# Kernel optimization log

Measured on AMD Instinct MI355X. Metric: run time of the kernel, lower is better.

The kernel has to match this reference:

```python
import jax, jax.numpy as jnp
import numpy as np

PS = 7        # pooled_size == conved_size
IMG = 300     # img_size
FMAP = 19     # feature map spatial size
SMAX = IMG // 16  # clamp max (18), matches torch long clamp(0, 300/16)
EPS = 1e-5


def _bn(x, g, b, m, v):
    scale = (g * jax.lax.rsqrt(v + EPS))[None, :, None, None]
    return x * scale + (b - m * g * jax.lax.rsqrt(v + EPS))[None, :, None, None]


def _conv(x, W, b=None, pad=1):
    y = jax.lax.conv_general_dilated(x, W, (1, 1), [(pad, pad), (pad, pad)],
                                     dimension_numbers=('NCHW', 'OIHW', 'NCHW'))
    if b is not None:
        y = y + b[None, :, None, None]
    return y


def _adaptive_w(lo, hi):
    # Per-ROI adaptive-avg-pool weights over the full 19-wide axis.
    # lo, hi: [B,R] inclusive crop bounds. Returns [B,R,PS,FMAP].
    H = hi - lo + 1                                  # crop length per ROI
    i = jnp.arange(PS)
    s = (i[None, None, :] * H[..., None]) // PS      # bin start (floor)
    e = -((-(i[None, None, :] + 1) * H[..., None]) // PS)  # bin end (ceil)
    rows = jnp.arange(FMAP)
    start = lo[..., None, None] + s[..., None]
    stop = lo[..., None, None] + e[..., None]
    mask = (rows >= start) & (rows < stop)
    denom = jnp.maximum(e - s, 1).astype(jnp.float32)[..., None]
    return mask.astype(jnp.float32) / denom


def setup_inputs() -> dict:
    key = jax.random.key(0)
    ks = jax.random.split(key, 6)
    B, R = 8, 128
    return {
        'roi_proposal': jax.random.uniform(ks[0], (B, 1, R, 5), dtype=jnp.float32),
        'features': jax.random.normal(ks[1], (B, 1024, FMAP, FMAP), dtype=jnp.float32),
        'W1': jax.random.normal(ks[2], (256, 1024, 3, 3), dtype=jnp.float32) * 0.02,
        'b1': jnp.zeros((256,), jnp.float32),
        'g1': jnp.ones((256,), jnp.float32),
        'be1': jnp.zeros((256,), jnp.float32),
        'm1': jnp.zeros((256,), jnp.float32),
        'v1': jnp.ones((256,), jnp.float32),
        'W2': jax.random.normal(ks[3], (256, 256, 3, 3), jnp.float32) * 0.05,
        'b2': jnp.zeros((256,), jnp.float32),
        'g2': jnp.ones((256,), jnp.float32),
        'be2': jnp.zeros((256,), jnp.float32),
        'm2': jnp.zeros((256,), jnp.float32),
        'v2': jnp.ones((256,), jnp.float32),
        'W3': jax.random.normal(ks[4], (32, 256, 1, 1), jnp.float32) * 0.1,
        'g3': jnp.ones((32,), jnp.float32),
        'be3': jnp.zeros((32,), jnp.float32),
        'm3': jnp.zeros((32,), jnp.float32),
        'v3': jnp.ones((32,), jnp.float32),
    }


def reference(roi_proposal, features, W1, b1, g1, be1, m1, v1,
              W2, b2, g2, be2, m2, v2, W3, g3, be3, m3, v3):
    # rois[..., 1:] * img_size / 16, then trunc to long (coords are >= 0)
    rl = (roi_proposal[:, 0, :, 1:] * (IMG / 16.0)).astype(jnp.int32)  # [B,R,4]
    c = jnp.clip(rl, 0, SMAX)
    xmin, ymin, xmax, ymax = c[..., 0], c[..., 1], c[..., 2], c[..., 3]
    valid = (xmax > xmin) & (ymax > ymin)                              # [B,R]
    B, R = valid.shape

    # fused crop + adaptive avg pool as two small pooling matmuls per ROI
    Wy = _adaptive_w(ymin, ymax)   # [B,R,7,19]
    Wx = _adaptive_w(xmin, xmax)   # [B,R,7,19]
    pooled = jnp.einsum('brph,bchw,brqw->brcpq', Wy, features, Wx)     # [B,R,1024,7,7]

    x = pooled.reshape(B * R, 1024, PS, PS)
    x = jax.nn.relu(_bn(_conv(x, W1, b1), g1, be1, m1, v1))
    x = jax.nn.relu(_bn(_conv(x, W2, b2), g2, be2, m2, v2))
    x = jax.nn.relu(_bn(_conv(x, W3, None, pad=0), g3, be3, m3, v3))
    out = x.reshape(B, R, 32, PS, PS) * valid[:, :, None, None, None]

    # compact valid ROIs to the front per batch (stable), invalid slots zeroed
    perm = jnp.argsort((~valid).astype(jnp.int32), axis=1, stable=True)
    out_c = jax.vmap(lambda o, p: o[p])(out, perm)                     # [B,R,32,7,7]
    er = rl.astype(jnp.float32) * (16.0 / IMG) * valid[..., None]
    er_c = jax.vmap(lambda o, p: o[p])(er, perm)[:, None]              # [B,1,R,4]
    keep_count = valid.sum(axis=1).astype(jnp.int32)                   # [B]
    return er_c, out_c, keep_count
```

## Files before the change

### kernel.cpp

```cpp
#include <hip/hip_runtime.h>
#include <cstddef>
#include <cstdint>

typedef unsigned short u16;
typedef unsigned int u32;
typedef __attribute__((ext_vector_type(8))) short short8;
typedef __attribute__((ext_vector_type(4))) float f32x4;

#define NB 8
#define NR 128
#define NPOS 49
#define EPSV 1e-5f
#define NSLOT 512

#define OUT_OC   4096
#define OUT_KEEP 1609728

static constexpr size_t OFF_META = 256;
static constexpr size_t OFF_KEEP = 33024;
static constexpr size_t OFF_W1Q  = 40960;
static constexpr size_t OFF_W2Q  = OFF_W1Q + 4718592;
static constexpr size_t OFF_W3   = OFF_W2Q + 1179648;
static constexpr size_t OFF_X1S  = OFF_W3  + 32768;
static constexpr size_t OFF_AP   = OFF_X1S + 13107200;
static constexpr size_t WS_NEED  = OFF_AP  + 51380224;

static __device__ __forceinline__ u16 f2bf(float f) {
  union { float f; u32 u; } x; x.f = f;
  u32 r = 0x7fffu + ((x.u >> 16) & 1u);
  return (u16)((x.u + r) >> 16);
}

__global__ void k_setup(const float* __restrict__ roi, int* __restrict__ cnt,
                        int* __restrict__ meta, int* __restrict__ keepd,
                        float* __restrict__ out)
{
  int b = blockIdx.x, t = threadIdx.x;
  __shared__ int sval[128], spre[129];
  const float* rp = roi + (size_t)(b * NR + t) * 5;
  int rl[4], cl[4];
#pragma unroll
  for (int j = 0; j < 4; ++j) {
    rl[j] = (int)(rp[1 + j] * 18.75f);
    cl[j] = min(max(rl[j], 0), 18);
  }
  int valid = (cl[2] > cl[0]) && (cl[3] > cl[1]) ? 1 : 0;
  sval[t] = valid;
  __syncthreads();
  if (t == 0) {
    int s = 0;
    for (int i = 0; i < 128; ++i) { spre[i] = s; s += sval[i]; }
    spre[128] = s;
    keepd[b] = s;
    out[OUT_KEEP + b] = (float)s;
  }
  __syncthreads();
  int keep = spre[128];
  if (valid) {
    int dst = spre[t];
    int slot = atomicAdd(cnt, 1);
    int* mt = meta + slot * 8;
    mt[0] = b; mt[1] = dst;
    mt[2] = cl[1]; mt[3] = cl[3];
    mt[4] = cl[0]; mt[5] = cl[2];
#pragma unroll
    for (int j = 0; j < 4; ++j)
      out[(size_t)(b * NR + dst) * 4 + j] = (float)rl[j] * (16.0f / 300.0f);
  }
  if (t >= keep) {
#pragma unroll
    for (int j = 0; j < 4; ++j) out[(size_t)(b * NR + t) * 4 + j] = 0.f;
  }
}

__global__ __launch_bounds__(256) void k_int(const float* __restrict__ feat, float* __restrict__ S)
{
  int b = blockIdx.x, cg = blockIdx.y;
  __shared__ float F[64 * 361];
  int tid = threadIdx.x;
  const float* fb = feat + ((size_t)b * 1024 + cg * 64) * 361;
#pragma unroll 1
  for (int i = tid; i < 64 * 361; i += 256) F[i] = fb[i];
  __syncthreads();
  if (tid < 64) {
    int ch = tid;
    const float* fp = F + ch * 361;
    float* Sp = S + (size_t)b * 400 * 1024 + cg * 64 + ch;
    float prev[20];
#pragma unroll
    for (int w = 0; w < 20; ++w) { prev[w] = 0.f; Sp[(size_t)w * 1024] = 0.f; }
    for (int h = 0; h < 19; ++h) {
      float run = 0.f;
      float* Sr = Sp + (size_t)(h + 1) * 20 * 1024;
      Sr[0] = 0.f;
#pragma unroll
      for (int w = 0; w < 19; ++w) {
        run += fp[h * 19 + w];
        float v = run + prev[w + 1];
        Sr[(size_t)(w + 1) * 1024] = v;
        prev[w + 1] = v;
      }
    }
  }
}

__device__ __forceinline__ void packw_body(const float* __restrict__ W, u16* __restrict__ wq,
                                           int IC, int c, int og)
{
  __shared__ float F[32 * 576];
  int tid = threadIdx.x, oc0 = og * 32;
#pragma unroll 1
  for (int i = tid; i < 18432; i += 256) {
    int ocr = i / 576, r = i - ocr * 576;
    F[i] = W[(size_t)(oc0 + ocr) * IC * 9 + c * 576 + r];
  }
  __syncthreads();
#pragma unroll 1
  for (int w = tid; w < 18432; w += 256) {
    int j = w & 7, lane = (w >> 3) & 63, rest = w >> 9;
    int ntr = rest & 1, kk = rest >> 1;
    int k9i = kk >> 1, ks = kk & 1;
    int ocr = ntr * 16 + (lane & 15);
    int icr = ks * 32 + ((lane >> 4) & 3) * 8 + j;
    int bid_ = (c * 9 + k9i) * 2 + ks;
    wq[((size_t)bid_ * 1024 + (oc0 / 16 + ntr) * 64 + lane) * 8 + j] = f2bf(F[ocr * 576 + icr * 9 + k9i]);
  }
}
__global__ __launch_bounds__(256) void k_prep(
    const float* __restrict__ W1, const float* __restrict__ W2, const float* __restrict__ W3,
    u16* __restrict__ w1q, u16* __restrict__ w2q, u16* __restrict__ w3q)
{
  if (blockIdx.z == 0) { packw_body(W1, w1q, 1024, blockIdx.x, blockIdx.y); return; }
  if (blockIdx.x < 4)  { packw_body(W2, w2q, 256, blockIdx.x, blockIdx.y); return; }
  if (blockIdx.x == 4 && blockIdx.y == 0) {
    for (int i = threadIdx.x; i < 8192; i += 256) {
      int oc = i >> 8, ic = i & 255;
      int kk = ic >> 5;
      int lane = ((ic >> 3) & 3) * 16 + (oc & 15);
      int nt16 = oc >> 4;
      int j = ic & 7;
      w3q[((size_t)((kk * 2 + nt16) * 64) + lane) * 8 + j] = f2bf(W3[i]);
    }
  }
}

__global__ __launch_bounds__(256) void k_pool(
    const int* __restrict__ cnt, const int* __restrict__ meta,
    const float* __restrict__ S, u16* __restrict__ Apool)
{
  int cv = *cnt; if (cv > NSLOT) cv = NSLOT;
  int slot = blockIdx.x;
  if (slot >= cv) return;
  const int* mt_ = meta + slot * 8;
  int b = mt_[0], ylo = mt_[2], yhi = mt_[3], xlo = mt_[4], xhi = mt_[5];
  int Hy = yhi - ylo + 1, Hx = xhi - xlo + 1;
  const float* Sb = S + (size_t)b * 400 * 1024;
  u16* Ap = Apool + (size_t)slot * 50176;
  int base = blockIdx.y * 25088, end = base + 25088;
  int tid = threadIdx.x;
#pragma unroll 1
  for (int t0 = base + tid; t0 < end; t0 += 1024) {
#pragma unroll
    for (int u = 0; u < 4; ++u) {
      int t = t0 + u * 256;
      if (t < end) {
        int ch = t & 63, r = t >> 6;
        int bin = r % 49, c = r / 49;
        int p = bin / 7, q = bin - 7 * p;
        int sy = (p * Hy) / 7, ey = ((p + 1) * Hy + 6) / 7;
        int sx = (q * Hx) / 7, ex = ((q + 1) * Hx + 6) / 7;
        int y0 = ylo + sy, y1 = ylo + ey, x0 = xlo + sx, x1 = xlo + ex;
        const float* Sc = Sb + c * 64 + ch;
        float v = Sc[(size_t)(y1 * 20 + x1) * 1024] - Sc[(size_t)(y0 * 20 + x1) * 1024]
                - Sc[(size_t)(y1 * 20 + x0) * 1024] + Sc[(size_t)(y0 * 20 + x0) * 1024];
        v /= (float)((ey - sy) * (ex - sx));
        Ap[(size_t)c * 3136 + bin * 64 + ch] = f2bf(v);
      }
    }
  }
}

template<int STR>
__device__ __forceinline__ void build_aoffp(int n, int kq, int (&aoffp)[9][2]) {
#pragma unroll
  for (int t9 = 0; t9 < 9; ++t9) {
    int off[4];
#pragma unroll
    for (int mt = 0; mt < 4; ++mt) {
      int lm = mt * 16 + n;
      int mv = lm < 49;
      int lm2 = mv ? lm : 0;
      int p = lm2 / 7, q = lm2 - 7 * p;
      int ky = t9 / 3, kx = t9 - 3 * (t9 / 3);
      int ry = p + ky - 1, rx = q + kx - 1;
      int ok = mv && ry >= 0 && ry < 7 && rx >= 0 && rx < 7;
      int rr = ok ? ry * 7 + rx : 49;
      off[mt] = rr * STR + kq * 8;
    }
    aoffp[t9][0] = (off[0] & 0xFFFF) | (off[1] << 16);
    aoffp[t9][1] = (off[2] & 0xFFFF) | (off[3] << 16);
  }
}

#define A1STR 1032
__global__ __launch_bounds__(512) void k_conv1(
    const int* __restrict__ cnt, const u16* __restrict__ Apool, const u16* __restrict__ wq,
    const float* __restrict__ bb, const float* __restrict__ gg, const float* __restrict__ bec,
    const float* __restrict__ mm, const float* __restrict__ vv,
    u16* __restrict__ x1)
{
  int cv = *cnt; if (cv > NSLOT) cv = NSLOT;
  int slot = blockIdx.x, ocq = blockIdx.y;
  if (slot >= cv) return;

  __shared__ __align__(16) char smem[103424];
  u16* panel = (u16*)smem;
  float* red = (float*)smem;

  int tid = threadIdx.x, lane = tid & 63, wave = tid >> 6;
  int n = lane & 15, kq = lane >> 4;

  for (int i = tid; i < A1STR / 2; i += 512) ((u32*)(panel + 49 * A1STR))[i] = 0;
  const uint4* src = (const uint4*)(Apool + (size_t)slot * 50176);
#pragma unroll 1
  for (int i = tid; i < 6272; i += 512) {
    int c = i / 392, rem = i - c * 392, bin = rem >> 3, ch8 = rem & 7;
    *(uint4*)(panel + bin * A1STR + c * 64 + ch8 * 8) = src[i];
  }

  int aoffp[9][2];
  build_aoffp<A1STR>(n, kq, aoffp);
  f32x4 acc[4][4];
#pragma unroll
  for (int i = 0; i < 4; ++i)
#pragma unroll
    for (int j = 0; j < 4; ++j) acc[i][j] = (f32x4){0.f, 0.f, 0.f, 0.f};

  const u16* pf = wq + (size_t)(ocq * 4) * 512 + (size_t)lane * 8 + (size_t)(wave * 2) * 18 * 8192;
  short8 bbuf[3][4];
#pragma unroll
  for (int r2 = 0; r2 < 3; ++r2)
#pragma unroll
    for (int nt = 0; nt < 4; ++nt) bbuf[r2][nt] = *(const short8*)(pf + (size_t)r2 * 8192 + nt * 512);
  pf += (size_t)3 * 8192;

  __syncthreads();

#pragma unroll 1
  for (int ci = 0; ci < 2; ++ci) {
    int cb = (wave * 2 + ci) * 64;
#pragma unroll
    for (int kk = 0; kk < 18; ++kk) {
      int t9 = kk >> 1, ks = kk & 1;
      short8 bfr[4], afr[4];
#pragma unroll
      for (int nt = 0; nt < 4; ++nt) bfr[nt] = bbuf[kk % 3][nt];
#pragma unroll
      for (int nt = 0; nt < 4; ++nt) bbuf[kk % 3][nt] = *(const short8*)(pf + nt * 512);
      pf += 8192;
      int coff = cb + ks * 32;
      int o0 = (aoffp[t9][0] & 0xFFFF) + coff, o1 = (int)((u32)aoffp[t9][0] >> 16) + coff;
      int o2 = (aoffp[t9][1] & 0xFFFF) + coff, o3 = (int)((u32)aoffp[t9][1] >> 16) + coff;
      afr[0] = *(const short8*)(panel + o0); afr[1] = *(const short8*)(panel + o1);
      afr[2] = *(const short8*)(panel + o2); afr[3] = *(const short8*)(panel + o3);
#pragma unroll
      for (int mt = 0; mt < 4; ++mt)
#pragma unroll
        for (int nt = 0; nt < 4; ++nt)
          acc[mt][nt] = __builtin_amdgcn_mfma_f32_16x16x32_bf16(afr[mt], bfr[nt], acc[mt][nt], 0, 0, 0);
    }
  }

  __syncthreads();
#pragma unroll
  for (int nt = 0; nt < 4; ++nt)
#pragma unroll
    for (int mt = 0; mt < 4; ++mt)
#pragma unroll
      for (int r = 0; r < 4; ++r) {
        int m = mt * 16 + kq * 4 + r;
        if (m < 49) red[wave * 3136 + m * 64 + nt * 16 + n] = acc[mt][nt][r];
      }
  __syncthreads();
#pragma unroll 1
  for (int i = tid; i < 3136; i += 512) {
    float s = 0.f;
#pragma unroll
    for (int w8 = 0; w8 < 8; ++w8) s += red[w8 * 3136 + i];
    int oc = ocq * 64 + (i & 63);
    float sc = gg[oc] * rsqrtf(vv[oc] + EPSV);
    float sh = (bb[oc] - mm[oc]) * sc + bec[oc];
    float y = fmaf(s, sc, sh);
    x1[((size_t)slot * 4 + ocq) * 3136 + i] = f2bf(y > 0.f ? y : 0.f);
  }
}

__global__ __launch_bounds__(512) void k_conv23(
    const int* __restrict__ cnt, const int* __restrict__ meta, const int* __restrict__ keepd,
    const u16* __restrict__ x1, const u16* __restrict__ w2q, const u16* __restrict__ w3q,
    const float* __restrict__ b2, const float* __restrict__ g2, const float* __restrict__ be2,
    const float* __restrict__ m2, const float* __restrict__ v2,
    const float* __restrict__ g3, const float* __restrict__ be3,
    const float* __restrict__ m3, const float* __restrict__ v3,
    float* __restrict__ out)
{
  int cv = *cnt; if (cv > NSLOT) cv = NSLOT;
  int slot = blockIdx.x;
  int tid = threadIdx.x;
  if (slot >= cv) {
    int nfill = NSLOT - cv;
#pragma unroll 1
    for (int j = slot - cv; j < 1024; j += nfill) {
      int b = j >> 7, dd = j & 127;
      if (dd >= keepd[b]) {
        float* o = out + OUT_OC + (size_t)(b * NR + dd) * 1568;
        for (int t = tid; t < 1568; t += 512) o[t] = 0.f;
      }
    }
    return;
  }
  const int* mt_ = meta + slot * 8;
  int b = mt_[0], dst = mt_[1];

  __shared__ __align__(16) char smem[77600];
  u16*   panels = (u16*)smem;
  float* red    = (float*)smem;
  u16*   xp     = (u16*)(smem + 51200);
  float* red3   = (float*)smem;

  int lane = tid & 63, wave = tid >> 6;
  int nt4 = wave & 3, kh = wave >> 2;
  int n = lane & 15, kq = lane >> 4;

  for (int i = tid; i < 4 * 36; i += 512) {
    int sp = i / 36, w2 = i - sp * 36;
    ((u32*)(panels + sp * 3600 + 49 * 72))[w2] = 0;
  }
  const u16* xs = x1 + (size_t)slot * 4 * 3136;
#pragma unroll 1
  for (int t = tid; t < 1568; t += 512) {
    int c = t / 392, e = t - c * 392;
    uint4 v = *((const uint4*)(xs + (size_t)c * 3136) + e);
    *(uint4*)(panels + (size_t)c * 3600 + (e >> 3) * 72 + (e & 7) * 8) = v;
  }

  int aoffp[9][2];
  build_aoffp<72>(n, kq, aoffp);
  f32x4 acc[4][4];
#pragma unroll
  for (int i = 0; i < 4; ++i)
#pragma unroll
    for (int j = 0; j < 4; ++j) acc[i][j] = (f32x4){0.f, 0.f, 0.f, 0.f};

  const u16* pf = w2q + (size_t)(nt4 * 4) * 512 + (size_t)lane * 8 + (size_t)(kh * 36) * 8192;
  short8 bbuf[3][4];
#pragma unroll
  for (int r2 = 0; r2 < 3; ++r2)
#pragma unroll
    for (int nt = 0; nt < 4; ++nt) bbuf[r2][nt] = *(const short8*)(pf + (size_t)r2 * 8192 + nt * 512);
  pf += (size_t)3 * 8192;

  __syncthreads();

#pragma unroll 1
  for (int ci = 0; ci < 2; ++ci) {
    const u16* P = panels + (size_t)(kh * 2 + ci) * 3600;
#pragma unroll
    for (int kk = 0; kk < 18; ++kk) {
      int t9 = kk >> 1, ks = kk & 1;
      short8 bfr[4], afr[4];
#pragma unroll
      for (int nt = 0; nt < 4; ++nt) bfr[nt] = bbuf[kk % 3][nt];
#pragma unroll
      for (int nt = 0; nt < 4; ++nt) bbuf[kk % 3][nt] = *(const short8*)(pf + nt * 512);
      pf += 8192;
      int coff = ks * 32;
      int o0 = (aoffp[t9][0] & 0xFFFF) + coff, o1 = (int)((u32)aoffp[t9][0] >> 16) + coff;
      int o2 = (aoffp[t9][1] & 0xFFFF) + coff, o3 = (int)((u32)aoffp[t9][1] >> 16) + coff;
      afr[0] = *(const short8*)(P + o0); afr[1] = *(const short8*)(P + o1);
      afr[2] = *(const short8*)(P + o2); afr[3] = *(const short8*)(P + o3);
#pragma unroll
      for (int mt = 0; mt < 4; ++mt)
#pragma unroll
        for (int nt = 0; nt < 4; ++nt)
          acc[mt][nt] = __builtin_amdgcn_mfma_f32_16x16x32_bf16(afr[mt], bfr[nt], acc[mt][nt], 0, 0, 0);
    }
  }
  __syncthreads();

  if (kh == 1) {
#pragma unroll
    for (int nt = 0; nt < 4; ++nt)
#pragma unroll
      for (int mt = 0; mt < 4; ++mt)
#pragma unroll
        for (int r = 0; r < 4; ++r) {
          int m = mt * 16 + kq * 4 + r;
          if (m < 49) red[((size_t)nt4 * 49 + m) * 64 + nt * 16 + n] = acc[mt][nt][r];
        }
  }
  __syncthreads();
  if (kh == 0) {
#pragma unroll
    for (int nt = 0; nt < 4; ++nt) {
      int oc = nt4 * 64 + nt * 16 + n;
      float sc = g2[oc] * rsqrtf(v2[oc] + EPSV);
      float sh = (b2[oc] - m2[oc]) * sc + be2[oc];
#pragma unroll
      for (int mt = 0; mt < 4; ++mt)
#pragma unroll
        for (int r = 0; r < 4; ++r) {
          int m = mt * 16 + kq * 4 + r;
          if (m < 49) {
            float y = acc[mt][nt][r] + red[((size_t)nt4 * 49 + m) * 64 + nt * 16 + n];
            y = fmaf(y, sc, sh);
            xp[m * 264 + oc] = f2bf(y > 0.f ? y : 0.f);
          }
        }
    }
  }
  if (wave == 4) {
    for (int i = lane; i < 132; i += 64) ((u32*)(xp + 49 * 264))[i] = 0;
  }
  __syncthreads();

  f32x4 a3[4][2];
#pragma unroll
  for (int mt = 0; mt < 4; ++mt) { a3[mt][0] = (f32x4){0,0,0,0}; a3[mt][1] = (f32x4){0,0,0,0}; }
  const u16* b3 = w3q + ((size_t)(wave * 2) * 64 + lane) * 8;
  short8 bf0 = *(const short8*)(b3);
  short8 bf1 = *(const short8*)(b3 + 512);
#pragma unroll
  for (int mt = 0; mt < 4; ++mt) {
    int m = mt * 16 + n;
    int row = m < 49 ? m : 49;
    short8 a = *(const short8*)(xp + row * 264 + wave * 32 + kq * 8);
    a3[mt][0] = __builtin_amdgcn_mfma_f32_16x16x32_bf16(a, bf0, a3[mt][0], 0, 0, 0);
    a3[mt][1] = __builtin_amdgcn_mfma_f32_16x16x32_bf16(a, bf1, a3[mt][1], 0, 0, 0);
  }
#pragma unroll
  for (int nt = 0; nt < 2; ++nt)
#pragma unroll
    for (int mt = 0; mt < 4; ++mt)
#pragma unroll
      for (int r = 0; r < 4; ++r) {
        int m = mt * 16 + kq * 4 + r;
        if (m < 49) red3[((size_t)wave * 49 + m) * 32 + nt * 16 + n] = a3[mt][nt][r];
      }
  __syncthreads();

  size_t ob = OUT_OC + ((size_t)(b * NR + dst) * 32) * 49;
#pragma unroll 1
  for (int t = tid; t < 1568; t += 512) {
    int m = t >> 5, oc = t & 31;
    float s = 0.f;
#pragma unroll
    for (int w8 = 0; w8 < 8; ++w8) s += red3[((size_t)w8 * 49 + m) * 32 + oc];
    float sc = g3[oc] * rsqrtf(v3[oc] + EPSV);
    float y = fmaf(s, sc, be3[oc] - m3[oc] * sc);
    out[ob + (size_t)oc * 49 + m] = y > 0.f ? y : 0.f;
  }
}

extern "C" void kernel_launch(void* const* d_in, const int* in_sizes, int n_in,
                              void* d_out, int out_size, void* d_ws, size_t ws_size,
                              hipStream_t stream)
{
  (void)in_sizes; (void)n_in; (void)out_size;
  if (ws_size < WS_NEED) return;

  const float* roi  = (const float*)d_in[0];
  const float* feat = (const float*)d_in[1];
  const float* W1   = (const float*)d_in[2];
  const float* b1   = (const float*)d_in[3];
  const float* g1   = (const float*)d_in[4];
  const float* be1  = (const float*)d_in[5];
  const float* m1   = (const float*)d_in[6];
  const float* v1   = (const float*)d_in[7];
  const float* W2   = (const float*)d_in[8];
  const float* b2   = (const float*)d_in[9];
  const float* g2   = (const float*)d_in[10];
  const float* be2  = (const float*)d_in[11];
  const float* m2   = (const float*)d_in[12];
  const float* v2   = (const float*)d_in[13];
  const float* W3   = (const float*)d_in[14];
  const float* g3   = (const float*)d_in[15];
  const float* be3  = (const float*)d_in[16];
  const float* m3   = (const float*)d_in[17];
  const float* v3   = (const float*)d_in[18];

  char* ws    = (char*)d_ws;
  int*  cnt   = (int*)ws;
  int*  meta  = (int*)(ws + OFF_META);
  int*  keepd = (int*)(ws + OFF_KEEP);
  u16*  w1q   = (u16*)(ws + OFF_W1Q);
  u16*  w2q   = (u16*)(ws + OFF_W2Q);
  u16*  w3q   = (u16*)(ws + OFF_W3);
  float* S    = (float*)(ws + OFF_X1S);
  u16*  x1    = (u16*)(ws + OFF_X1S);
  u16*  Apool = (u16*)(ws + OFF_AP);
  float* out  = (float*)d_out;

  hipMemsetAsync(cnt, 0, 4, stream);

  k_int<<<dim3(NB, 16), 256, 0, stream>>>(feat, S);
  k_prep<<<dim3(16, 8, 2), 256, 0, stream>>>(W1, W2, W3, w1q, w2q, w3q);
  k_setup<<<NB, NR, 0, stream>>>(roi, cnt, meta, keepd, out);

  k_pool<<<dim3(NSLOT, 2), 256, 0, stream>>>(cnt, meta, S, Apool);
  k_conv1<<<dim3(NSLOT, 4), 512, 0, stream>>>(cnt, Apool, w1q, b1, g1, be1, m1, v1, x1);
  k_conv23<<<NSLOT, 512, 0, stream>>>(cnt, meta, keepd, x1, w2q, w3q,
                                      b2, g2, be2, m2, v2, g3, be3, m3, v3, out);
}
```

Measured before the change: 305.2 us.

## Batch four ROIs per conv1 block with double-buffered channel panels; merge prep kernels

Conv1 blocks now handle four ROI slots each. Waves are split into two K-halves by four ROIs, so every weight fragment loaded from global memory is reused across four ROIs instead of one. Input channel panels are streamed in 64-channel chunks through double-buffered shared memory, with register prefetch overlapping the MFMA loop. The cross-wave reduction shrinks to a single pairwise add. The integral-image, weight-pack and ROI setup kernels are merged into one launch to cut launch overhead. The cost is more shared-memory traffic per block and fewer blocks, which may lower occupancy.

```diff
diff --git a/kernel.cpp b/kernel.cpp
--- a/kernel.cpp
+++ b/kernel.cpp
@@ -31,52 +31,9 @@
   return (u16)((x.u + r) >> 16);
 }
 
-__global__ void k_setup(const float* __restrict__ roi, int* __restrict__ cnt,
-                        int* __restrict__ meta, int* __restrict__ keepd,
-                        float* __restrict__ out)
-{
-  int b = blockIdx.x, t = threadIdx.x;
-  __shared__ int sval[128], spre[129];
-  const float* rp = roi + (size_t)(b * NR + t) * 5;
-  int rl[4], cl[4];
-#pragma unroll
-  for (int j = 0; j < 4; ++j) {
-    rl[j] = (int)(rp[1 + j] * 18.75f);
-    cl[j] = min(max(rl[j], 0), 18);
-  }
-  int valid = (cl[2] > cl[0]) && (cl[3] > cl[1]) ? 1 : 0;
-  sval[t] = valid;
-  __syncthreads();
-  if (t == 0) {
-    int s = 0;
-    for (int i = 0; i < 128; ++i) { spre[i] = s; s += sval[i]; }
-    spre[128] = s;
-    keepd[b] = s;
-    out[OUT_KEEP + b] = (float)s;
-  }
-  __syncthreads();
-  int keep = spre[128];
-  if (valid) {
-    int dst = spre[t];
-    int slot = atomicAdd(cnt, 1);
-    int* mt = meta + slot * 8;
-    mt[0] = b; mt[1] = dst;
-    mt[2] = cl[1]; mt[3] = cl[3];
-    mt[4] = cl[0]; mt[5] = cl[2];
-#pragma unroll
-    for (int j = 0; j < 4; ++j)
-      out[(size_t)(b * NR + dst) * 4 + j] = (float)rl[j] * (16.0f / 300.0f);
-  }
-  if (t >= keep) {
-#pragma unroll
-    for (int j = 0; j < 4; ++j) out[(size_t)(b * NR + t) * 4 + j] = 0.f;
-  }
-}
-
-__global__ __launch_bounds__(256) void k_int(const float* __restrict__ feat, float* __restrict__ S)
-{
-  int b = blockIdx.x, cg = blockIdx.y;
-  __shared__ float F[64 * 361];
+__device__ __forceinline__ void int_body(const float* __restrict__ feat, float* __restrict__ S,
+                                         int b, int cg, float* F)
+{
   int tid = threadIdx.x;
   const float* fb = feat + ((size_t)b * 1024 + cg * 64) * 361;
 #pragma unroll 1
@@ -105,9 +62,8 @@
 }
 
 __device__ __forceinline__ void packw_body(const float* __restrict__ W, u16* __restrict__ wq,
-                                           int IC, int c, int og)
-{
-  __shared__ float F[32 * 576];
+                                           int IC, int c, int og, float* F)
+{
   int tid = threadIdx.x, oc0 = og * 32;
 #pragma unroll 1
   for (int i = tid; i < 18432; i += 256) {
@@ -126,13 +82,20 @@
     wq[((size_t)bid_ * 1024 + (oc0 / 16 + ntr) * 64 + lane) * 8 + j] = f2bf(F[ocr * 576 + icr * 9 + k9i]);
   }
 }
+
 __global__ __launch_bounds__(256) void k_prep(
+    const float* __restrict__ feat, float* __restrict__ S,
     const float* __restrict__ W1, const float* __restrict__ W2, const float* __restrict__ W3,
-    u16* __restrict__ w1q, u16* __restrict__ w2q, u16* __restrict__ w3q)
-{
-  if (blockIdx.z == 0) { packw_body(W1, w1q, 1024, blockIdx.x, blockIdx.y); return; }
-  if (blockIdx.x < 4)  { packw_body(W2, w2q, 256, blockIdx.x, blockIdx.y); return; }
-  if (blockIdx.x == 4 && blockIdx.y == 0) {
+    u16* __restrict__ w1q, u16* __restrict__ w2q, u16* __restrict__ w3q,
+    const float* __restrict__ roi, int* __restrict__ cnt,
+    int* __restrict__ meta, int* __restrict__ keepd, float* __restrict__ out)
+{
+  __shared__ float SH[23104];
+  int bx = blockIdx.x;
+  if (bx < 128) { int_body(feat, S, bx >> 4, bx & 15, SH); return; }
+  if (bx < 256) { packw_body(W1, w1q, 1024, (bx - 128) >> 3, (bx - 128) & 7, SH); return; }
+  if (bx < 288) { packw_body(W2, w2q, 256, (bx - 256) >> 3, (bx - 256) & 7, SH); return; }
+  if (bx == 288) {
     for (int i = threadIdx.x; i < 8192; i += 256) {
       int oc = i >> 8, ic = i & 255;
       int kk = ic >> 5;
@@ -140,6 +103,48 @@
       int nt16 = oc >> 4;
       int j = ic & 7;
       w3q[((size_t)((kk * 2 + nt16) * 64) + lane) * 8 + j] = f2bf(W3[i]);
+    }
+    return;
+  }
+  int b = bx - 289, t = threadIdx.x;
+  int* sval = (int*)SH;
+  int* spre = sval + 128;
+  int rl[4], cl[4], valid = 0;
+  if (t < 128) {
+    const float* rp = roi + (size_t)(b * NR + t) * 5;
+#pragma unroll
+    for (int j = 0; j < 4; ++j) {
+      rl[j] = (int)(rp[1 + j] * 18.75f);
+      cl[j] = min(max(rl[j], 0), 18);
+    }
+    valid = (cl[2] > cl[0]) && (cl[3] > cl[1]) ? 1 : 0;
+    sval[t] = valid;
+  }
+  __syncthreads();
+  if (t == 0) {
+    int s = 0;
+    for (int i = 0; i < 128; ++i) { spre[i] = s; s += sval[i]; }
+    spre[128] = s;
+    keepd[b] = s;
+    out[OUT_KEEP + b] = (float)s;
+  }
+  __syncthreads();
+  if (t < 128) {
+    int keep = spre[128];
+    if (valid) {
+      int dst = spre[t];
+      int slot = atomicAdd(cnt, 1);
+      int* mt = meta + slot * 8;
+      mt[0] = b; mt[1] = dst;
+      mt[2] = cl[1]; mt[3] = cl[3];
+      mt[4] = cl[0]; mt[5] = cl[2];
+#pragma unroll
+      for (int j = 0; j < 4; ++j)
+        out[(size_t)(b * NR + dst) * 4 + j] = (float)rl[j] * (16.0f / 300.0f);
+    }
+    if (t >= keep) {
+#pragma unroll
+      for (int j = 0; j < 4; ++j) out[(size_t)(b * NR + t) * 4 + j] = 0.f;
     }
   }
 }
@@ -202,7 +207,6 @@
   }
 }
 
-#define A1STR 1032
 __global__ __launch_bounds__(512) void k_conv1(
     const int* __restrict__ cnt, const u16* __restrict__ Apool, const u16* __restrict__ wq,
     const float* __restrict__ bb, const float* __restrict__ gg, const float* __restrict__ bec,
@@ -210,88 +214,130 @@
     u16* __restrict__ x1)
 {
   int cv = *cnt; if (cv > NSLOT) cv = NSLOT;
-  int slot = blockIdx.x, ocq = blockIdx.y;
-  if (slot >= cv) return;
-
-  __shared__ __align__(16) char smem[103424];
-  u16* panel = (u16*)smem;
-  float* red = (float*)smem;
+  int slot0 = blockIdx.x * 4, ocq = blockIdx.y;
+  if (slot0 >= cv) return;
+
+  __shared__ __align__(16) u16 panels[16 * 3600];
+  float* red = (float*)panels;
 
   int tid = threadIdx.x, lane = tid & 63, wave = tid >> 6;
+  int kh = wave >> 2, roi4 = wave & 3;
   int n = lane & 15, kq = lane >> 4;
 
-  for (int i = tid; i < A1STR / 2; i += 512) ((u32*)(panel + 49 * A1STR))[i] = 0;
-  const uint4* src = (const uint4*)(Apool + (size_t)slot * 50176);
-#pragma unroll 1
-  for (int i = tid; i < 6272; i += 512) {
-    int c = i / 392, rem = i - c * 392, bin = rem >> 3, ch8 = rem & 7;
-    *(uint4*)(panel + bin * A1STR + c * 64 + ch8 * 8) = src[i];
+  for (int i = tid; i < 16 * 36; i += 512) {
+    int sp = i / 36, w2 = i - sp * 36;
+    ((u32*)(panels + sp * 3600 + 49 * 72))[w2] = 0;
   }
 
   int aoffp[9][2];
-  build_aoffp<A1STR>(n, kq, aoffp);
+  build_aoffp<72>(n, kq, aoffp);
   f32x4 acc[4][4];
 #pragma unroll
   for (int i = 0; i < 4; ++i)
 #pragma unroll
     for (int j = 0; j < 4; ++j) acc[i][j] = (f32x4){0.f, 0.f, 0.f, 0.f};
 
-  const u16* pf = wq + (size_t)(ocq * 4) * 512 + (size_t)lane * 8 + (size_t)(wave * 2) * 18 * 8192;
-  short8 bbuf[3][4];
-#pragma unroll
-  for (int r2 = 0; r2 < 3; ++r2)
-#pragma unroll
-    for (int nt = 0; nt < 4; ++nt) bbuf[r2][nt] = *(const short8*)(pf + (size_t)r2 * 8192 + nt * 512);
-  pf += (size_t)3 * 8192;
-
-  __syncthreads();
-
-#pragma unroll 1
-  for (int ci = 0; ci < 2; ++ci) {
-    int cb = (wave * 2 + ci) * 64;
+  const u16* pf = wq + (size_t)(ocq * 4) * 512 + (size_t)lane * 8 + (size_t)(kh * 8) * 18 * 8192;
+  short8 bbuf[2][4];
+#pragma unroll
+  for (int nt = 0; nt < 4; ++nt) bbuf[0][nt] = *(const short8*)(pf + nt * 512);
+#pragma unroll
+  for (int nt = 0; nt < 4; ++nt) bbuf[1][nt] = *(const short8*)(pf + 8192 + nt * 512);
+  pf += (size_t)2 * 8192;
+
+  uint4 sbuf[7];
+  auto load_issue = [&](int ca, int cb) {
+#pragma unroll
+    for (int j = 0; j < 7; ++j) {
+      int t = tid + j * 512;
+      if (t < 3136) {
+        int khs = t >= 1568 ? 1 : 0;
+        int e2 = t - khs * 1568;
+        int rr = e2 / 392, e = e2 - rr * 392;
+        int c = khs ? cb : ca;
+        int sl = slot0 + rr; if (sl >= cv) sl = cv - 1;
+        sbuf[j] = *((const uint4*)(Apool + ((size_t)sl * 16 + c) * 3136) + e);
+      }
+    }
+  };
+  auto write_sbuf = [&](int B) {
+#pragma unroll
+    for (int j = 0; j < 7; ++j) {
+      int t = tid + j * 512;
+      if (t < 3136) {
+        int khs = t >= 1568 ? 1 : 0;
+        int e2 = t - khs * 1568;
+        int rr = e2 / 392, e = e2 - rr * 392;
+        *(uint4*)(panels + (size_t)((B * 2 + khs) * 4 + rr) * 3600 + (e >> 3) * 72 + (e & 7) * 8) = sbuf[j];
+      }
+    }
+  };
+
+  load_issue(0, 8);
+  write_sbuf(0);
+  __syncthreads();
+
+#pragma unroll 1
+  for (int i = 0; i < 8; ++i) {
+    if (i + 1 < 8) load_issue(i + 1, 9 + i);
+    const u16* P = panels + (size_t)(((i & 1) * 2 + kh) * 4 + roi4) * 3600;
 #pragma unroll
     for (int kk = 0; kk < 18; ++kk) {
       int t9 = kk >> 1, ks = kk & 1;
       short8 bfr[4], afr[4];
 #pragma unroll
-      for (int nt = 0; nt < 4; ++nt) bfr[nt] = bbuf[kk % 3][nt];
-#pragma unroll
-      for (int nt = 0; nt < 4; ++nt) bbuf[kk % 3][nt] = *(const short8*)(pf + nt * 512);
+      for (int nt = 0; nt < 4; ++nt) bfr[nt] = bbuf[kk & 1][nt];
+#pragma unroll
+      for (int nt = 0; nt < 4; ++nt) bbuf[kk & 1][nt] = *(const short8*)(pf + nt * 512);
       pf += 8192;
-      int coff = cb + ks * 32;
+      int coff = ks * 32;
       int o0 = (aoffp[t9][0] & 0xFFFF) + coff, o1 = (int)((u32)aoffp[t9][0] >> 16) + coff;
       int o2 = (aoffp[t9][1] & 0xFFFF) + coff, o3 = (int)((u32)aoffp[t9][1] >> 16) + coff;
-      afr[0] = *(const short8*)(panel + o0); afr[1] = *(const short8*)(panel + o1);
-      afr[2] = *(const short8*)(panel + o2); afr[3] = *(const short8*)(panel + o3);
+      afr[0] = *(const short8*)(P + o0); afr[1] = *(const short8*)(P + o1);
+      afr[2] = *(const short8*)(P + o2); afr[3] = *(const short8*)(P + o3);
 #pragma unroll
       for (int mt = 0; mt < 4; ++mt)
 #pragma unroll
         for (int nt = 0; nt < 4; ++nt)
           acc[mt][nt] = __builtin_amdgcn_mfma_f32_16x16x32_bf16(afr[mt], bfr[nt], acc[mt][nt], 0, 0, 0);
     }
-  }
-
-  __syncthreads();
-#pragma unroll
-  for (int nt = 0; nt < 4; ++nt)
-#pragma unroll
-    for (int mt = 0; mt < 4; ++mt)
-#pragma unroll
-      for (int r = 0; r < 4; ++r) {
-        int m = mt * 16 + kq * 4 + r;
-        if (m < 49) red[wave * 3136 + m * 64 + nt * 16 + n] = acc[mt][nt][r];
-      }
-  __syncthreads();
-#pragma unroll 1
-  for (int i = tid; i < 3136; i += 512) {
-    float s = 0.f;
-#pragma unroll
-    for (int w8 = 0; w8 < 8; ++w8) s += red[w8 * 3136 + i];
-    int oc = ocq * 64 + (i & 63);
-    float sc = gg[oc] * rsqrtf(vv[oc] + EPSV);
-    float sh = (bb[oc] - mm[oc]) * sc + bec[oc];
-    float y = fmaf(s, sc, sh);
-    x1[((size_t)slot * 4 + ocq) * 3136 + i] = f2bf(y > 0.f ? y : 0.f);
+    if (i + 1 < 8) write_sbuf((i + 1) & 1);
+    __syncthreads();
+  }
+
+  if (kh == 1) {
+#pragma unroll
+    for (int nt = 0; nt < 4; ++nt)
+#pragma unroll
+      for (int mt = 0; mt < 4; ++mt)
+#pragma unroll
+        for (int r = 0; r < 4; ++r) {
+          int m = mt * 16 + kq * 4 + r;
+          if (m < 49) red[((size_t)roi4 * 49 + m) * 64 + nt * 16 + n] = acc[mt][nt][r];
+        }
+  }
+  __syncthreads();
+  if (kh == 0) {
+    int slot = slot0 + roi4;
+    if (slot < cv) {
+#pragma unroll
+      for (int nt = 0; nt < 4; ++nt) {
+        int oc = ocq * 64 + nt * 16 + n;
+        float sc = gg[oc] * rsqrtf(vv[oc] + EPSV);
+        float sh = (bb[oc] - mm[oc]) * sc + bec[oc];
+#pragma unroll
+        for (int mt = 0; mt < 4; ++mt)
+#pragma unroll
+          for (int r = 0; r < 4; ++r) {
+            int m = mt * 16 + kq * 4 + r;
+            if (m < 49) {
+              float y = acc[mt][nt][r] + red[((size_t)roi4 * 49 + m) * 64 + nt * 16 + n];
+              y = fmaf(y, sc, sh);
+              x1[((size_t)slot * 4 + ocq) * 3136 + m * 64 + nt * 16 + n] = f2bf(y > 0.f ? y : 0.f);
+            }
+          }
+      }
+    }
   }
 }
 
@@ -503,12 +549,10 @@
 
   hipMemsetAsync(cnt, 0, 4, stream);
 
-  k_int<<<dim3(NB, 16), 256, 0, stream>>>(feat, S);
-  k_prep<<<dim3(16, 8, 2), 256, 0, stream>>>(W1, W2, W3, w1q, w2q, w3q);
-  k_setup<<<NB, NR, 0, stream>>>(roi, cnt, meta, keepd, out);
-
+  k_prep<<<297, 256, 0, stream>>>(feat, S, W1, W2, W3, w1q, w2q, w3q,
+                                  roi, cnt, meta, keepd, out);
   k_pool<<<dim3(NSLOT, 2), 256, 0, stream>>>(cnt, meta, S, Apool);
-  k_conv1<<<dim3(NSLOT, 4), 512, 0, stream>>>(cnt, Apool, w1q, b1, g1, be1, m1, v1, x1);
+  k_conv1<<<dim3(NSLOT / 4, 4), 512, 0, stream>>>(cnt, Apool, w1q, b1, g1, be1, m1, v1, x1);
   k_conv23<<<NSLOT, 512, 0, stream>>>(cnt, meta, keepd, x1, w2q, w3q,
                                       b2, g2, be2, m2, v2, g3, be3, m3, v3, out);
 }
```

Result: slower. 313.4 us (+2.7%).
